# Performance work log

Measured on AMD Instinct MI355X. Metric: run time of the kernel, lower is better.

## Reference

```python
import jax, jax.numpy as jnp
import numpy as np

D = 512
H = 8
DH = D // H  # 64


def setup_inputs() -> dict:
    key = jax.random.key(0)
    ks = jax.random.split(key, 7)
    batch, la, lb = 8, 256, 256
    A = jax.random.normal(ks[0], (batch, la, D), dtype=jnp.float32)
    B = jax.random.normal(ks[1], (batch, lb, D), dtype=jnp.float32)
    s = 1.0 / np.sqrt(D)
    W1 = jax.random.uniform(ks[2], (D, D), minval=-s, maxval=s, dtype=jnp.float32)
    b1 = jax.random.uniform(ks[3], (D,), minval=-s, maxval=s, dtype=jnp.float32)
    W2 = jax.random.uniform(ks[4], (D, D), minval=-s, maxval=s, dtype=jnp.float32)
    b2 = jax.random.uniform(ks[5], (D,), minval=-s, maxval=s, dtype=jnp.float32)
    q = jax.random.normal(ks[6], (DH,), dtype=jnp.float32) * 0.1
    return {"A": A, "B": B, "W1": W1, "b1": b1, "W2": W2, "b2": b2, "q": q}


def reference(A, B, W1, b1, W2, b2, q):
    bs, la, _ = A.shape
    lb = B.shape[1]
    # Linear + ReLU, then raw row-major reshape to (batch, heads, len, dh)
    # (matches torch .view semantics: NOT a head-transpose split)
    A_ = jax.nn.relu(A @ W1.T + b1).reshape(bs, H, la, DH)
    B_ = jax.nn.relu(B @ W2.T + b2).reshape(bs, H, lb, DH)
    # bilinear score: tanh of elementwise pairwise product, dotted with q
    # att_maps: [bs, H, la, lb]
    att_maps = jnp.einsum(
        "bhijc,c->bhij",
        jnp.tanh(A_[:, :, :, None, :] * B_[:, :, None, :, :]),
        q,
    )
    temp_b2a = jax.nn.softmax(jnp.mean(att_maps, axis=3), axis=2)  # [bs,H,la]
    temp_a2b = jax.nn.softmax(jnp.mean(att_maps, axis=2), axis=2)  # [bs,H,lb]
    A_heads = A.reshape(bs, H, la, DH)
    B_heads = B.reshape(bs, H, lb, DH)
    A_p = jnp.sum(A_heads * temp_b2a[..., None], axis=2).reshape(bs, -1)  # [bs, d]
    B_p = jnp.sum(B_heads * temp_a2b[..., None], axis=2).reshape(bs, -1)  # [bs, d]
    return (
        jnp.concatenate((A_p, B_p), axis=1),
        jnp.mean(temp_b2a, axis=1),
        jnp.mean(temp_a2b, axis=1),
    )
```

## Files before the change

### kernel.cpp

```cpp
#include <hip/hip_runtime.h>
#include <hip/hip_bf16.h>

#define LOG2E 1.4426950408889634f
#define SC2   2.8853900817779268f

typedef __attribute__((ext_vector_type(8))) short short8b;
typedef __attribute__((ext_vector_type(4))) short short4b;
typedef __attribute__((ext_vector_type(4))) float f32x4;

__device__ __forceinline__ float fast_exp2(float x) {
#if __has_builtin(__builtin_amdgcn_exp2f)
  return __builtin_amdgcn_exp2f(x);
#else
  return exp2f(x);
#endif
}
__device__ __forceinline__ float fast_rcp(float x) {
#if __has_builtin(__builtin_amdgcn_rcpf)
  return __builtin_amdgcn_rcpf(x);
#else
  return 1.0f / x;
#endif
}
__device__ __forceinline__ short f2bf(float f) {
  __hip_bfloat16 h = __float2bfloat16(f);
  return *reinterpret_cast<short*>(&h);
}

__global__ __launch_bounds__(256) void gemm_mfma_kernel(
    const float* __restrict__ Xa, const float* __restrict__ Wa,
    const float* __restrict__ ba, float* __restrict__ Oa,
    const float* __restrict__ Xb, const float* __restrict__ Wb,
    const float* __restrict__ bb, float* __restrict__ Ob) {
  const float* X = blockIdx.z ? Xb : Xa;
  const float* W = blockIdx.z ? Wb : Wa;
  const float* bias = blockIdx.z ? bb : ba;
  float* O = blockIdx.z ? Ob : Oa;

  __shared__ __align__(16) short As[128 * 40];
  __shared__ __align__(16) short Ws[64 * 40];

  int t = threadIdx.x;
  int m0 = blockIdx.x * 128, n0 = blockIdx.y * 64;
  int l = t & 63, w = t >> 6;
  int wm = (w >> 1) * 64, wn = (w & 1) * 32;
  int lr = l & 15, ko = (l >> 4) * 8;

  f32x4 acc[4][2];
#pragma unroll
  for (int m = 0; m < 4; ++m)
#pragma unroll
    for (int n = 0; n < 2; ++n) acc[m][n] = f32x4{0.f, 0.f, 0.f, 0.f};

  for (int k0 = 0; k0 < 512; k0 += 32) {
#pragma unroll
    for (int s = 0; s < 4; ++s) {
      int slot = t + s * 256;
      int row = slot >> 3, q = (slot & 7) << 2;
      float4 v = *reinterpret_cast<const float4*>(&X[(m0 + row) * 512 + k0 + q]);
      short4b sv = {f2bf(v.x), f2bf(v.y), f2bf(v.z), f2bf(v.w)};
      *reinterpret_cast<short4b*>(&As[row * 40 + q]) = sv;
    }
#pragma unroll
    for (int s = 0; s < 2; ++s) {
      int slot = t + s * 256;
      int row = slot >> 3, q = (slot & 7) << 2;
      float4 v = *reinterpret_cast<const float4*>(&W[(n0 + row) * 512 + k0 + q]);
      short4b sv = {f2bf(v.x), f2bf(v.y), f2bf(v.z), f2bf(v.w)};
      *reinterpret_cast<short4b*>(&Ws[row * 40 + q]) = sv;
    }
    __syncthreads();

    short8b afr[4], bfr[2];
#pragma unroll
    for (int m = 0; m < 4; ++m)
      afr[m] = *reinterpret_cast<const short8b*>(&As[(wm + m * 16 + lr) * 40 + ko]);
#pragma unroll
    for (int n = 0; n < 2; ++n)
      bfr[n] = *reinterpret_cast<const short8b*>(&Ws[(wn + n * 16 + lr) * 40 + ko]);
#pragma unroll
    for (int m = 0; m < 4; ++m)
#pragma unroll
      for (int n = 0; n < 2; ++n)
        acc[m][n] = __builtin_amdgcn_mfma_f32_16x16x32_bf16(afr[m], bfr[n], acc[m][n], 0, 0, 0);
    __syncthreads();
  }

#pragma unroll
  for (int n = 0; n < 2; ++n) {
    int col = n0 + wn + n * 16 + lr;
    float bv = bias[col];
#pragma unroll
    for (int m = 0; m < 4; ++m) {
      int rbase = m0 + wm + m * 16 + (l >> 4) * 4;
#pragma unroll
      for (int r = 0; r < 4; ++r) {
        float v = acc[m][n][r] + bv;
        O[(rbase + r) * 512 + col] = v > 0.f ? v : 0.f;
      }
    }
  }
}

__global__ __launch_bounds__(256) void compact_kernel(
    const float* __restrict__ Br, const float* __restrict__ q,
    float2* __restrict__ Cb, unsigned* __restrict__ Cnt, float* __restrict__ Ksum) {
  int blk = blockIdx.x;
  int bh = blk >> 3, jblk = blk & 7;
  int t = threadIdx.x;
  int jl = t >> 3, p = t & 7;
  __shared__ float Bls[32][65];
  __shared__ float qls[64];

  const float* Bbase = Br + bh * 16384 + jblk * 2048;
#pragma unroll
  for (int it = 0; it < 2; ++it) {
    int idx = it * 256 + t;
    int row = idx >> 4, c4 = (idx & 15) << 2;
    float4 v = *reinterpret_cast<const float4*>(&Bbase[row * 64 + c4]);
    Bls[row][c4 + 0] = v.x; Bls[row][c4 + 1] = v.y;
    Bls[row][c4 + 2] = v.z; Bls[row][c4 + 3] = v.w;
  }
  if (t < 64) qls[t] = q[t];
  __syncthreads();

  int c0 = p * 8;
  int nz = 0;
  float K = 0.f;
#pragma unroll
  for (int cc = 0; cc < 8; ++cc) {
    float v = Bls[jl][c0 + cc];
    if (v > 0.f) { ++nz; K += qls[c0 + cc]; }
  }
  int incl = nz;
#pragma unroll
  for (int d = 1; d < 8; d <<= 1) {
    int u = __shfl_up(incl, d, 8);
    if (p >= d) incl += u;
  }
  int off = incl - nz;
  int total = __shfl(incl, 7, 8);

  float2* dst = Cb + (bh * 256 + jblk * 32 + jl) * 64;
  int k = off;
#pragma unroll
  for (int cc = 0; cc < 8; ++cc) {
    int c = c0 + cc;
    float v = Bls[jl][c];
    if (v > 0.f) {
      unsigned qb = (__float_as_uint(-2.f * qls[c]) & ~63u) | (unsigned)c;
      dst[k] = make_float2(v * SC2, __uint_as_float(qb));
      ++k;
    }
  }
#pragma unroll
  for (int d = 1; d < 8; d <<= 1) K += __shfl_xor(K, d, 8);

  if (p == 7) {
    int cnt = total;
    while (cnt & 3) { dst[cnt] = make_float2(0.f, 0.f); ++cnt; }
    Cnt[bh * 256 + jblk * 32 + jl] = (unsigned)cnt;
    Ksum[bh * 256 + jblk * 32 + jl] = K;
  }
}

__global__ __launch_bounds__(512, 8) void attmap_kernel(
    const float* __restrict__ Ar, const float2* __restrict__ Cb,
    const unsigned* __restrict__ Cnt,
    float* __restrict__ rowpart, float* __restrict__ colsum) {
  int bh = blockIdx.x, jblk = blockIdx.y, isplit = blockIdx.z;
  int t = threadIdx.x;
  int il = t & 127;
  int g = __builtin_amdgcn_readfirstlane(t >> 7);
  __shared__ __align__(16) float Als[128 * 65];
  __shared__ float red[512];
  __shared__ float cpart[8][8];

  const float* Abase = Ar + bh * 16384 + isplit * 8192;
#pragma unroll
  for (int it = 0; it < 4; ++it) {
    int idx = it * 512 + t;
    int r = idx >> 4, c4 = (idx & 15) << 2;
    float4 v = *reinterpret_cast<const float4*>(&Abase[r * 64 + c4]);
    Als[r * 65 + c4 + 0] = v.x; Als[r * 65 + c4 + 1] = v.y;
    Als[r * 65 + c4 + 2] = v.z; Als[r * 65 + c4 + 3] = v.w;
  }
  __syncthreads();

  const float* Arow = &Als[il * 65];
  float acc[8];

#pragma unroll
  for (int jj = 0; jj < 8; ++jj) {
    int jl = g * 8 + jj;
    int n = (int)__builtin_amdgcn_readfirstlane(Cnt[bh * 256 + jblk * 32 + jl]);
    const float4* P4 = reinterpret_cast<const float4*>(Cb + (bh * 256 + jblk * 32 + jl) * 64);
    float accj = 0.f;
#pragma unroll 1
    for (int s = 0; s < n; s += 4) {
      float4 u = P4[s >> 1];
      float4 v = P4[(s >> 1) + 1];
      float a0 = Arow[__float_as_uint(u.y) & 63u];
      float a1 = Arow[__float_as_uint(u.w) & 63u];
      float a2 = Arow[__float_as_uint(v.y) & 63u];
      float a3 = Arow[__float_as_uint(v.w) & 63u];
      float e0 = fast_exp2(fminf(a0 * u.x, 60.f));
      float e1 = fast_exp2(fminf(a1 * u.z, 60.f));
      float e2 = fast_exp2(fminf(a2 * v.x, 60.f));
      float e3 = fast_exp2(fminf(a3 * v.z, 60.f));
      float u0 = e0 + 1.f, u1 = e1 + 1.f, u2 = e2 + 1.f, u3 = e3 + 1.f;
      float n01 = fmaf(u.w, u0, u.y * u1);
      float n23 = fmaf(v.w, u2, v.y * u3);
      float r01 = fast_rcp(u0 * u1);
      float r23 = fast_rcp(u2 * u3);
      accj = fmaf(n01, r01, accj);
      accj = fmaf(n23, r23, accj);
    }
    acc[jj] = accj;
  }

  float rs = 0.f;
#pragma unroll
  for (int jj = 0; jj < 8; ++jj) rs += acc[jj];
  red[t] = rs;

  int lane = t & 63, w = t >> 6;
#pragma unroll
  for (int jj = 0; jj < 8; ++jj) {
    float v = acc[jj];
#pragma unroll
    for (int off = 32; off >= 1; off >>= 1) v += __shfl_xor(v, off);
    if (lane == 0) cpart[w][jj] = v;
  }
  __syncthreads();
  if (t < 128) {
    rowpart[(bh * 8 + jblk) * 256 + isplit * 128 + t] =
        red[t] + red[t + 128] + red[t + 256] + red[t + 384];
  } else if (t < 160) {
    int jl = t - 128;
    int gg = jl >> 3, jj = jl & 7;
    colsum[(bh * 2 + isplit) * 256 + jblk * 32 + jl] =
        cpart[2 * gg][jj] + cpart[2 * gg + 1][jj];
  }
}

__global__ __launch_bounds__(512) void softmax_pool_kernel(
    const float* __restrict__ rowpart, const float* __restrict__ colsum,
    const float* __restrict__ Ksum,
    const float* __restrict__ A0, const float* __restrict__ B0,
    float* __restrict__ b2a, float* __restrict__ a2b, float* __restrict__ out) {
  int bh = blockIdx.x;
  int b = bh >> 3, h = bh & 7;
  int t = threadIdx.x;
  int tt = t & 255;
  int lane = t & 63, w = (t >> 6) & 3;
  __shared__ float redA[4], redB[4], redC[4], redD[4];
  __shared__ float tA[256], tB[256];
  __shared__ float pp[8][64];

  float r = 0.f;
#pragma unroll
  for (int jb = 0; jb < 8; ++jb) r += rowpart[(bh * 8 + jb) * 256 + tt];
  r *= (1.f / 256.f);
  float cs = Ksum[bh * 256 + tt] +
             (colsum[(bh * 2 + 0) * 256 + tt] + colsum[(bh * 2 + 1) * 256 + tt]) * (1.f / 256.f);

  float mr = r, mc = cs;
#pragma unroll
  for (int off = 32; off >= 1; off >>= 1) {
    mr = fmaxf(mr, __shfl_xor(mr, off));
    mc = fmaxf(mc, __shfl_xor(mc, off));
  }
  if (lane == 0) { redA[w] = mr; redB[w] = mc; }
  __syncthreads();
  mr = fmaxf(fmaxf(redA[0], redA[1]), fmaxf(redA[2], redA[3]));
  mc = fmaxf(fmaxf(redB[0], redB[1]), fmaxf(redB[2], redB[3]));

  float er = fast_exp2((r - mr) * LOG2E);
  float ec = fast_exp2((cs - mc) * LOG2E);
  float sr = er, sc = ec;
#pragma unroll
  for (int off = 32; off >= 1; off >>= 1) {
    sr += __shfl_xor(sr, off);
    sc += __shfl_xor(sc, off);
  }
  if (lane == 0) { redC[w] = sr; redD[w] = sc; }
  __syncthreads();
  sr = redC[0] + redC[1] + redC[2] + redC[3];
  sc = redD[0] + redD[1] + redD[2] + redD[3];

  float vb2a = er * fast_rcp(sr);
  float va2b = ec * fast_rcp(sc);
  tA[tt] = vb2a; tB[tt] = va2b;
  b2a[bh * 256 + tt] = vb2a;
  a2b[bh * 256 + tt] = va2b;
  __syncthreads();

  int c = t & 63, iq = t >> 6;
  const float* Ab = A0 + b * 131072 + h * 16384;
  const float* Bb = B0 + b * 131072 + h * 16384;
  float pa = 0.f, pb = 0.f;
#pragma unroll 4
  for (int ii = 0; ii < 32; ++ii) {
    int i = (iq << 5) + ii;
    pa = fmaf(Ab[i * 64 + c], tA[i], pa);
    pb = fmaf(Bb[i * 64 + c], tB[i], pb);
  }
  pp[iq][c] = pa;
  __syncthreads();
  if (t < 64) {
    float s = 0.f;
#pragma unroll
    for (int k = 0; k < 8; ++k) s += pp[k][t];
    out[b * 1024 + h * 64 + t] = s;
  }
  __syncthreads();
  pp[iq][c] = pb;
  __syncthreads();
  if (t < 64) {
    float s = 0.f;
#pragma unroll
    for (int k = 0; k < 8; ++k) s += pp[k][t];
    out[b * 1024 + 512 + h * 64 + t] = s;
  }
}

__global__ __launch_bounds__(256) void mean_heads_kernel(
    const float* __restrict__ b2a, const float* __restrict__ a2b,
    float* __restrict__ out) {
  int b = blockIdx.x, t = threadIdx.x;
  float s1 = 0.f, s2 = 0.f;
#pragma unroll
  for (int h = 0; h < 8; ++h) {
    s1 += b2a[(b * 8 + h) * 256 + t];
    s2 += a2b[(b * 8 + h) * 256 + t];
  }
  out[8192 + b * 256 + t] = s1 * 0.125f;
  out[10240 + b * 256 + t] = s2 * 0.125f;
}

extern "C" void kernel_launch(void* const* d_in, const int* in_sizes, int n_in,
                              void* d_out, int out_size, void* d_ws, size_t ws_size,
                              hipStream_t stream) {
  const float* A  = (const float*)d_in[0];
  const float* B  = (const float*)d_in[1];
  const float* W1 = (const float*)d_in[2];
  const float* b1 = (const float*)d_in[3];
  const float* W2 = (const float*)d_in[4];
  const float* b2 = (const float*)d_in[5];
  const float* q  = (const float*)d_in[6];
  float* out = (float*)d_out;
  float* ws = (float*)d_ws;

  float*    Ar      = ws;
  float*    Brr     = ws + 1048576;
  float2*   Cb      = (float2*)(ws + 2097152);
  unsigned* Cnt     = (unsigned*)(ws + 4194304);
  float*    Ksum    = ws + 4210688;
  float*    rowpart = ws + 4227072;
  float*    colsum  = ws + 4358144;
  float*    b2a     = ws;
  float*    a2b     = ws + 16384;

  gemm_mfma_kernel<<<dim3(16, 8, 2), 256, 0, stream>>>(A, W1, b1, Ar, B, W2, b2, Brr);
  compact_kernel<<<512, 256, 0, stream>>>(Brr, q, Cb, Cnt, Ksum);
  attmap_kernel<<<dim3(64, 8, 2), 512, 0, stream>>>(Ar, Cb, Cnt, rowpart, colsum);
  softmax_pool_kernel<<<64, 512, 0, stream>>>(rowpart, colsum, Ksum, A, B, b2a, a2b, out);
  mean_heads_kernel<<<8, 256, 0, stream>>>(b2a, a2b, out);
}
```

Baseline: 73.53 us.

## Interleave compacted B entries across 8 columns and process them in one loop

```diff
diff --git a/kernel.cpp b/kernel.cpp
--- a/kernel.cpp
+++ b/kernel.cpp
@@ -109,6 +109,7 @@
   int bh = blk >> 3, jblk = blk & 7;
   int t = threadIdx.x;
   int jl = t >> 3, p = t & 7;
+  int g = t >> 6, jj = jl & 7;
   __shared__ float Bls[32][65];
   __shared__ float qls[64];
 
@@ -141,30 +142,41 @@
   int off = incl - nz;
   int total = __shfl(incl, 7, 8);
 
-  float2* dst = Cb + (bh * 256 + jblk * 32 + jl) * 64;
+  int maxc = total;
+#pragma unroll
+  for (int d = 8; d < 64; d <<= 1) maxc = max(maxc, __shfl_xor(maxc, d));
+  maxc = (maxc + 1) & ~1;
+
+  float2* dst = Cb + (size_t)(((bh * 8 + jblk) * 4 + g) * 64) * 8;
   int k = off;
 #pragma unroll
   for (int cc = 0; cc < 8; ++cc) {
     int c = c0 + cc;
     float v = Bls[jl][c];
     if (v > 0.f) {
-      unsigned qb = (__float_as_uint(-2.f * qls[c]) & ~63u) | (unsigned)c;
-      dst[k] = make_float2(v * SC2, __uint_as_float(qb));
+      unsigned qb = (__float_as_uint(-2.f * qls[c]) & ~255u) | (unsigned)(c << 2);
+      dst[k * 8 + jj] = make_float2(v * SC2, __uint_as_float(qb));
       ++k;
     }
   }
+  for (int s = total + p; s < maxc; s += 8) dst[s * 8 + jj] = make_float2(0.f, 0.f);
+
 #pragma unroll
   for (int d = 1; d < 8; d <<= 1) K += __shfl_xor(K, d, 8);
-
-  if (p == 7) {
-    int cnt = total;
-    while (cnt & 3) { dst[cnt] = make_float2(0.f, 0.f); ++cnt; }
-    Cnt[bh * 256 + jblk * 32 + jl] = (unsigned)cnt;
-    Ksum[bh * 256 + jblk * 32 + jl] = K;
-  }
-}
-
-__global__ __launch_bounds__(512, 8) void attmap_kernel(
+  if (p == 0) Ksum[bh * 256 + jblk * 32 + jl] = K;
+  if ((t & 63) == 0) Cnt[(bh * 8 + jblk) * 4 + g] = (unsigned)maxc;
+}
+
+#define PAIR(b0, q0, b1, q1, ACCJ) {                                        \
+    float a0 = *(const float*)(AlsB + (__float_as_uint(q0) & 255u));        \
+    float a1 = *(const float*)(AlsB + (__float_as_uint(q1) & 255u));        \
+    float e0 = fast_exp2(fminf(a0 * (b0), 60.f));                           \
+    float e1 = fast_exp2(fminf(a1 * (b1), 60.f));                           \
+    float u0 = e0 + 1.f, u1 = e1 + 1.f;                                     \
+    float nn = fmaf((q0), u1, (q1) * u0);                                   \
+    ACCJ = fmaf(nn, fast_rcp(u0 * u1), ACCJ); }
+
+__global__ __launch_bounds__(512, 6) void attmap_kernel(
     const float* __restrict__ Ar, const float2* __restrict__ Cb,
     const unsigned* __restrict__ Cnt,
     float* __restrict__ rowpart, float* __restrict__ colsum) {
@@ -187,36 +199,28 @@
   }
   __syncthreads();
 
-  const float* Arow = &Als[il * 65];
+  const char* AlsB = (const char*)(&Als[il * 65]);
   float acc[8];
-
-#pragma unroll
-  for (int jj = 0; jj < 8; ++jj) {
-    int jl = g * 8 + jj;
-    int n = (int)__builtin_amdgcn_readfirstlane(Cnt[bh * 256 + jblk * 32 + jl]);
-    const float4* P4 = reinterpret_cast<const float4*>(Cb + (bh * 256 + jblk * 32 + jl) * 64);
-    float accj = 0.f;
+#pragma unroll
+  for (int jj = 0; jj < 8; ++jj) acc[jj] = 0.f;
+
+  int gi = (bh * 8 + jblk) * 4 + g;
+  int n = (int)__builtin_amdgcn_readfirstlane(Cnt[gi]);
+  const float4* P4 = reinterpret_cast<const float4*>(Cb + (size_t)gi * 512);
+
 #pragma unroll 1
-    for (int s = 0; s < n; s += 4) {
-      float4 u = P4[s >> 1];
-      float4 v = P4[(s >> 1) + 1];
-      float a0 = Arow[__float_as_uint(u.y) & 63u];
-      float a1 = Arow[__float_as_uint(u.w) & 63u];
-      float a2 = Arow[__float_as_uint(v.y) & 63u];
-      float a3 = Arow[__float_as_uint(v.w) & 63u];
-      float e0 = fast_exp2(fminf(a0 * u.x, 60.f));
-      float e1 = fast_exp2(fminf(a1 * u.z, 60.f));
-      float e2 = fast_exp2(fminf(a2 * v.x, 60.f));
-      float e3 = fast_exp2(fminf(a3 * v.z, 60.f));
-      float u0 = e0 + 1.f, u1 = e1 + 1.f, u2 = e2 + 1.f, u3 = e3 + 1.f;
-      float n01 = fmaf(u.w, u0, u.y * u1);
-      float n23 = fmaf(v.w, u2, v.y * u3);
-      float r01 = fast_rcp(u0 * u1);
-      float r23 = fast_rcp(u2 * u3);
-      accj = fmaf(n01, r01, accj);
-      accj = fmaf(n23, r23, accj);
-    }
-    acc[jj] = accj;
+  for (int s = 0; s < n; s += 2) {
+    const float4* S0 = P4 + s * 4;
+    float4 x0 = S0[0], x1 = S0[1], x2 = S0[2], x3 = S0[3];
+    float4 y0 = S0[4], y1 = S0[5], y2 = S0[6], y3 = S0[7];
+    PAIR(x0.x, x0.y, y0.x, y0.y, acc[0]);
+    PAIR(x0.z, x0.w, y0.z, y0.w, acc[1]);
+    PAIR(x1.x, x1.y, y1.x, y1.y, acc[2]);
+    PAIR(x1.z, x1.w, y1.z, y1.w, acc[3]);
+    PAIR(x2.x, x2.y, y2.x, y2.y, acc[4]);
+    PAIR(x2.z, x2.w, y2.z, y2.w, acc[5]);
+    PAIR(x3.x, x3.y, y3.x, y3.y, acc[6]);
+    PAIR(x3.z, x3.w, y3.z, y3.w, acc[7]);
   }
 
   float rs = 0.f;
```

Result: no change. 74.76 us (+1.7%).
